# Performance work log

Measured on AMD Instinct MI355X. Metric: run time of the kernel, lower is better.

Reference implementation:

```python
import math
import jax, jax.numpy as jnp
import numpy as np

NUM_BUCKETS = 32
MAX_DISTANCE = 128
HEADS = 16
D_MODEL = 1024
SEQ = 1024
BATCH = 4
SCALE = (D_MODEL // HEADS) ** -0.5  # applied ONLY to the relative-position bias, per the source


def _rel_pos_bucket_causal(seq_len):
    """Causal T5 relative-position bucket: ret[i, j] for query i, key j."""
    pos = jnp.arange(seq_len)
    # rel_pos = k - q ; n = -rel_pos = q - k, clamped at 0 (causal branch)
    n = jnp.maximum(pos[:, None] - pos[None, :], 0)
    max_exact = NUM_BUCKETS // 2  # 16
    # log-spaced buckets for large distances; guard n>=1 to avoid log(0)
    val_large = max_exact + (
        jnp.log(jnp.maximum(n, 1).astype(jnp.float32) / max_exact)
        / math.log(MAX_DISTANCE / max_exact)
        * (NUM_BUCKETS - max_exact)
    ).astype(jnp.int32)
    val_large = jnp.minimum(val_large, NUM_BUCKETS - 1)
    return jnp.where(n < max_exact, n, val_large)  # [i, j] int32


def setup_inputs() -> dict:
    key = jax.random.key(0)
    ks = jax.random.split(key, 6)
    s = 0.02
    return {
        "x": jax.random.normal(ks[0], (BATCH, SEQ, D_MODEL), jnp.float32),
        "Wq": jax.random.normal(ks[1], (D_MODEL, D_MODEL), jnp.float32) * s,
        "bq": jnp.zeros((D_MODEL,), jnp.float32),
        "Wk": jax.random.normal(ks[2], (D_MODEL, D_MODEL), jnp.float32) * s,
        "bk": jnp.zeros((D_MODEL,), jnp.float32),
        "Wv": jax.random.normal(ks[3], (D_MODEL, D_MODEL), jnp.float32) * s,
        "bv": jnp.zeros((D_MODEL,), jnp.float32),
        "Wo": jax.random.normal(ks[4], (D_MODEL, D_MODEL), jnp.float32) * s,
        "bo": jnp.zeros((D_MODEL,), jnp.float32),
        "rel_emb": jax.random.normal(ks[5], (NUM_BUCKETS, HEADS), jnp.float32) * s,
    }


def reference(x, Wq, bq, Wk, bk, Wv, bv, Wo, bo, rel_emb):
    b, n, d = x.shape
    h, hd = HEADS, d // HEADS
    # projections (torch Linear: x @ W^T + b)
    q = (x @ Wq.T + bq).reshape(b, n, h, hd).transpose(0, 2, 1, 3)  # bhnd
    k = (x @ Wk.T + bk).reshape(b, n, h, hd).transpose(0, 2, 1, 3)
    v = (x @ Wv.T + bv).reshape(b, n, h, hd).transpose(0, 2, 1, 3)
    # unscaled dot-product scores (module does not scale q.k)
    sim = jnp.einsum("bhid,bhjd->bhij", q, k)
    # T5 relative-position bias, scaled by head_dim^-0.5
    rp_bucket = _rel_pos_bucket_causal(n)            # [i, j]
    bias = rel_emb[rp_bucket]                        # [i, j, h]
    sim = sim + jnp.transpose(bias, (2, 0, 1)) * SCALE  # broadcast over batch
    # additive causal mask (-inf above diagonal)
    i = jnp.arange(n)
    causal = jnp.where(i[None, :] > i[:, None], -jnp.inf, 0.0).astype(sim.dtype)
    sim = sim + causal
    attn = jax.nn.softmax(sim, axis=-1)
    out = jnp.einsum("bhij,bhjd->bhid", attn, v)
    out = out.transpose(0, 2, 1, 3).reshape(b, n, d)
    return out @ Wo.T + bo
```

## Files before the change

### kernel.cpp

```cpp
#include <hip/hip_runtime.h>
#include <hip/hip_bf16.h>
#include <stdint.h>

#define B_   4
#define SEQ_ 1024
#define DM   1024
#define H_   16
#define HD   64

typedef __bf16 bf16;
typedef __bf16 bf16x8 __attribute__((ext_vector_type(8)));
typedef __bf16 bf16x4v __attribute__((ext_vector_type(4)));
typedef __bf16 bf16x2 __attribute__((ext_vector_type(2)));
typedef float  f32x4 __attribute__((ext_vector_type(4)));

__device__ __forceinline__ void gl_lds16(const void* g, void* s_uniform) {
    __builtin_amdgcn_global_load_lds(
        (const __attribute__((address_space(1))) uint32_t*)g,
        (__attribute__((address_space(3))) uint32_t*)s_uniform,
        16, 0, 0);
}

__global__ __launch_bounds__(256) void prep_kernel(
    const float* __restrict__ x, const float* __restrict__ Wq,
    const float* __restrict__ Wk, const float* __restrict__ Wv,
    const float* __restrict__ Wo, const float* __restrict__ rel,
    bf16* __restrict__ xb, bf16* __restrict__ wqkvb, bf16* __restrict__ wob,
    float* __restrict__ biasT)
{
    int tid = blockIdx.x * 256 + threadIdx.x;
    int stride = gridDim.x * 256;

    for (int i = tid; i < (B_*SEQ_*DM)/4; i += stride) {
        float4 v = ((const float4*)x)[i];
        bf16x4v o; o[0]=(bf16)v.x; o[1]=(bf16)v.y; o[2]=(bf16)v.z; o[3]=(bf16)v.w;
        ((bf16x4v*)xb)[i] = o;
    }
    for (int i = tid; i < (3*DM*DM)/4; i += stride) {
        int n = i >> 8, k4 = i & 255;
        const float* src = (n < 1024) ? Wq : (n < 2048) ? Wk : Wv;
        float4 v = ((const float4*)(src + (size_t)(n & 1023) * DM))[k4];
        bf16x4v o; o[0]=(bf16)v.x; o[1]=(bf16)v.y; o[2]=(bf16)v.z; o[3]=(bf16)v.w;
        ((bf16x4v*)wqkvb)[i] = o;
    }
    for (int i = tid; i < (DM*DM)/4; i += stride) {
        float4 v = ((const float4*)Wo)[i];
        bf16x4v o; o[0]=(bf16)v.x; o[1]=(bf16)v.y; o[2]=(bf16)v.z; o[3]=(bf16)v.w;
        ((bf16x4v*)wob)[i] = o;
    }
    for (int i = tid; i < H_ * SEQ_; i += stride) {
        int h = i >> 10, dist = i & 1023;
        int bkt;
        if (dist < 16) {
            bkt = dist;
        } else {
            float r = logf((float)dist * (1.0f/16.0f)) / logf(8.0f) * 16.0f;
            int vb = 16 + (int)r;
            bkt = vb > 31 ? 31 : vb;
        }
        biasT[i] = rel[bkt * H_ + h] * 0.125f;
    }
}

template<int NT>
__global__ __launch_bounds__(256, 3) void gemm_ring(
    const bf16* __restrict__ Ag, const bf16* __restrict__ Bg,
    bf16* __restrict__ qb, bf16* __restrict__ kb, bf16* __restrict__ vtb,
    const float* __restrict__ bq, const float* __restrict__ bk,
    const float* __restrict__ bv)
{
    __shared__ __align__(16) bf16 tile[3][256 * 32];

    const int t = threadIdx.x;
    const int lane = t & 63, w = t >> 6;
    const int wr = w >> 1, wc = w & 1;
    const int row_l = lane & 15;
    const int lg = lane >> 4;

    int xcd = blockIdx.x & 7;
    int idx = blockIdx.x >> 3;
    int ty = (xcd >> 1) * 8 + idx / 12;
    int tx = (xcd & 1) * 12 + idx % 12;
    const int m0 = ty * 128, n0 = tx * 128;

    f32x4 acc[4][4] = {};

    auto STAGE = [&](int buf, int kt) {
        bf16* dst = &tile[buf][0];
        #pragma unroll
        for (int i = 0; i < 4; ++i) {
            int e = i * 2048 + t * 8;
            int r = e >> 5;
            int csw = ((t & 3) ^ (r & 3)) << 3;
            const bf16* src = (r < 128)
                ? (Ag + (long)(m0 + r) * 1024 + kt * 32 + csw)
                : (Bg + (long)(n0 + r - 128) * 1024 + kt * 32 + csw);
            gl_lds16(src, dst + i * 2048 + w * 512);
        }
    };

    auto COMPUTE = [&](int buf) {
        const bf16* bp = &tile[buf][0];
        bf16x8 af[4], bfr[4];
        #pragma unroll
        for (int m = 0; m < 4; ++m) {
            int ra = wr * 64 + m * 16 + row_l;
            af[m] = *(const bf16x8*)&bp[ra * 32 + ((lg ^ (ra & 3)) << 3)];
        }
        #pragma unroll
        for (int n = 0; n < 4; ++n) {
            int rb = 128 + wc * 64 + n * 16 + row_l;
            bfr[n] = *(const bf16x8*)&bp[rb * 32 + ((lg ^ (rb & 3)) << 3)];
        }
        #pragma unroll
        for (int m = 0; m < 4; ++m)
            #pragma unroll
            for (int n = 0; n < 4; ++n)
                acc[m][n] = __builtin_amdgcn_mfma_f32_16x16x32_bf16(
                    af[m], bfr[n], acc[m][n], 0, 0, 0);
    };

    STAGE(0, 0); STAGE(1, 1);
    asm volatile("s_waitcnt vmcnt(4)" ::: "memory");
    __builtin_amdgcn_s_barrier();

    int cb = 0;
    for (int kt = 0; kt < NT; ++kt) {
        int sb = cb - 1; if (sb < 0) sb += 3;
        if (kt + 2 < NT) STAGE(sb, kt + 2);
        COMPUTE(cb);
        if (kt + 2 < NT) { asm volatile("s_waitcnt vmcnt(4)" ::: "memory"); }
        else             { asm volatile("s_waitcnt vmcnt(0)" ::: "memory"); }
        __builtin_amdgcn_s_barrier();
        cb = (cb + 1 == 3) ? 0 : cb + 1;
    }

    const int rbase = (lane >> 4) * 4;

    if (n0 < 2048) {
        #pragma unroll
        for (int m = 0; m < 4; ++m) {
            #pragma unroll
            for (int n = 0; n < 4; ++n) {
                #pragma unroll
                for (int g = 0; g < 4; ++g) {
                    int gm = m0 + wr * 64 + m * 16 + rbase + g;
                    int gn = n0 + wc * 64 + n * 16 + row_l;
                    int which = gn >> 10, nn = gn & 1023;
                    int h = nn >> 6, d = nn & 63;
                    int b = gm >> 10, s = gm & 1023;
                    float v = acc[m][n][g] + ((which == 0) ? bq[nn] : bk[nn]);
                    bf16 bv16 = (bf16)v;
                    if (which == 0)
                        qb[((long)(b*H_ + h)*SEQ_ + s)*HD + d] = bv16;
                    else
                        kb[((long)(b*H_ + h)*SEQ_ + s)*HD + d] = bv16;
                }
            }
        }
    } else {
        bf16* lt = &tile[0][0];
        #pragma unroll
        for (int m = 0; m < 4; ++m) {
            #pragma unroll
            for (int n = 0; n < 4; ++n) {
                int nl = wc * 64 + n * 16 + row_l;
                int mlb = wr * 64 + m * 16 + rbase;
                float bvv = bv[(n0 & 1023) + nl];
                #pragma unroll
                for (int g2 = 0; g2 < 2; ++g2) {
                    bf16x2 pk;
                    pk[0] = (bf16)(acc[m][n][2*g2]     + bvv);
                    pk[1] = (bf16)(acc[m][n][2*g2 + 1] + bvv);
                    int ml = mlb + 2 * g2;
                    int byte = nl * 256 + ((ml * 2) ^ ((nl & 15) << 4));
                    *(bf16x2*)((char*)lt + byte) = pk;
                }
            }
        }
        __syncthreads();
        {
            int nl = t >> 1, sc = t & 1;
            int nn = (n0 & 1023) + nl;
            int h = nn >> 6, d = nn & 63;
            int b = m0 >> 10, s0 = (m0 & 1023) + sc * 64;
            bf16* dst = vtb + ((long)(b*H_ + h)*HD + d)*SEQ_ + s0;
            #pragma unroll
            for (int i = 0; i < 8; ++i) {
                int byte = nl * 256 + ((sc * 128 + i * 16) ^ ((nl & 15) << 4));
                *(float4*)(dst + i * 8) = *(const float4*)((char*)lt + byte);
            }
        }
    }
}

template<int NT>
__global__ __launch_bounds__(256, 2) void gemm_ring_o(
    const bf16* __restrict__ Ag, const bf16* __restrict__ Bg,
    float* __restrict__ outp, const float* __restrict__ bo)
{
    __shared__ __align__(16) bf16 tile[3][192 * 32];

    const int t = threadIdx.x;
    const int lane = t & 63, w = t >> 6;
    const int wr = w >> 1, wc = w & 1;
    const int row_l = lane & 15;
    const int lg = lane >> 4;

    int xcd = blockIdx.x & 7;
    int idx = blockIdx.x >> 3;
    int ty = (xcd >> 1) * 8 + (idx >> 3);
    int tx = (xcd & 1) * 8 + (idx & 7);
    const int m0 = ty * 128, n0 = tx * 64;

    f32x4 acc[4][2] = {};

    auto STAGE = [&](int buf, int kt) {
        bf16* dst = &tile[buf][0];
        #pragma unroll
        for (int i = 0; i < 3; ++i) {
            int e = i * 2048 + t * 8;
            int r = e >> 5;
            int csw = ((t & 3) ^ (r & 3)) << 3;
            const bf16* src = (r < 128)
                ? (Ag + (long)(m0 + r) * 1024 + kt * 32 + csw)
                : (Bg + (long)(n0 + r - 128) * 1024 + kt * 32 + csw);
            gl_lds16(src, dst + i * 2048 + w * 512);
        }
    };

    auto COMPUTE = [&](int buf) {
        const bf16* bp = &tile[buf][0];
        bf16x8 af[4], bfr[2];
        #pragma unroll
        for (int m = 0; m < 4; ++m) {
            int ra = wr * 64 + m * 16 + row_l;
            af[m] = *(const bf16x8*)&bp[ra * 32 + ((lg ^ (ra & 3)) << 3)];
        }
        #pragma unroll
        for (int n = 0; n < 2; ++n) {
            int rb = 128 + wc * 32 + n * 16 + row_l;
            bfr[n] = *(const bf16x8*)&bp[rb * 32 + ((lg ^ (rb & 3)) << 3)];
        }
        #pragma unroll
        for (int m = 0; m < 4; ++m)
            #pragma unroll
            for (int n = 0; n < 2; ++n)
                acc[m][n] = __builtin_amdgcn_mfma_f32_16x16x32_bf16(
                    af[m], bfr[n], acc[m][n], 0, 0, 0);
    };

    STAGE(0, 0); STAGE(1, 1);
    asm volatile("s_waitcnt vmcnt(3)" ::: "memory");
    __builtin_amdgcn_s_barrier();

    int cb = 0;
    for (int kt = 0; kt < NT; ++kt) {
        int sb = cb - 1; if (sb < 0) sb += 3;
        if (kt + 2 < NT) STAGE(sb, kt + 2);
        COMPUTE(cb);
        if (kt + 2 < NT) { asm volatile("s_waitcnt vmcnt(3)" ::: "memory"); }
        else             { asm volatile("s_waitcnt vmcnt(0)" ::: "memory"); }
        __builtin_amdgcn_s_barrier();
        cb = (cb + 1 == 3) ? 0 : cb + 1;
    }

    const int rbase = (lane >> 4) * 4;
    #pragma unroll
    for (int m = 0; m < 4; ++m) {
        #pragma unroll
        for (int n = 0; n < 2; ++n) {
            #pragma unroll
            for (int g = 0; g < 4; ++g) {
                int gm = m0 + wr * 64 + m * 16 + rbase + g;
                int gn = n0 + wc * 32 + n * 16 + row_l;
                outp[(long)gm * DM + gn] = acc[m][n][g] + bo[gn];
            }
        }
    }
}

#define PSTRIDE 72

__global__ __launch_bounds__(256, 3) void attn_kernel(
    const bf16* __restrict__ Qb, const bf16* __restrict__ Kb,
    const bf16* __restrict__ Vtb, const float* __restrict__ biasT,
    bf16* __restrict__ AO)
{
    __shared__ __align__(16) bf16 Ks[2][64 * 64];
    __shared__ __align__(16) bf16 Vs[2][64 * 64];
    __shared__ __align__(16) bf16 Ps[4][16 * PSTRIDE];
    __shared__ float biasS[SEQ_];

    int t = threadIdx.x;
    int lane = t & 63, w = t >> 6;

    int bid = blockIdx.x;
    int xcd = bid & 7;
    int widx = bid >> 3;
    int g = xcd * 8 + (widx >> 3);
    int pair = widx & 7;
    int qt_lo = pair, qt_hi = 15 - pair;
    int h = g & 15, b = g >> 4;

    int row_l = lane & 15;
    int ksl = (lane >> 4) * 8;
    int rbase = (lane >> 4) * 4;

    ((float4*)biasS)[t] = ((const float4*)(biasT + (long)h * SEQ_))[t];

    const bf16* Kbase = Kb + (long)g * SEQ_ * HD;
    const bf16* Vbase = Vtb + (long)g * HD * SEQ_;

    const bf16* QpA = Qb + ((long)g * SEQ_ + qt_lo * 64 + w * 16) * HD;
    const bf16* QpB = Qb + ((long)g * SEQ_ + qt_hi * 64 + w * 16) * HD;
    bf16x8 qA0 = *(const bf16x8*)&QpA[row_l * HD + ksl];
    bf16x8 qA1 = *(const bf16x8*)&QpA[row_l * HD + 32 + ksl];
    bf16x8 qB0 = *(const bf16x8*)&QpB[row_l * HD + ksl];
    bf16x8 qB1 = *(const bf16x8*)&QpB[row_l * HD + 32 + ksl];

    f32x4 oaccA[4] = {}, oaccB[4] = {};
    float lA[4] = {0.f, 0.f, 0.f, 0.f}, lB[4] = {0.f, 0.f, 0.f, 0.f};
    int irA[4], irB[4];
    #pragma unroll
    for (int q = 0; q < 4; ++q) {
        irA[q] = qt_lo * 64 + w * 16 + rbase + q;
        irB[q] = qt_hi * 64 + w * 16 + rbase + q;
    }

    int srow = w * 8 + (lane >> 3);
    int csw  = ((lane & 7) ^ (lane >> 3)) * 8;

    {
        int jt = 0;
        #pragma unroll
        for (int i = 0; i < 2; ++i) {
            int r = i * 32 + srow;
            gl_lds16(Kbase + (long)(jt*64 + r) * HD + csw, &Ks[0][i*2048 + w*512]);
            gl_lds16(Vbase + (long)r * SEQ_ + jt*64 + csw, &Vs[0][i*2048 + w*512]);
        }
    }
    __syncthreads();

    int cur = 0;
    for (int jt = 0; jt <= qt_hi; ++jt) {
        if (jt < qt_hi) {
            int nb = cur ^ 1, jn = jt + 1;
            #pragma unroll
            for (int i = 0; i < 2; ++i) {
                int r = i * 32 + srow;
                gl_lds16(Kbase + (long)(jn*64 + r) * HD + csw, &Ks[nb][i*2048 + w*512]);
                gl_lds16(Vbase + (long)r * SEQ_ + jn*64 + csw, &Vs[nb][i*2048 + w*512]);
            }
        }
        bool dolo = (jt <= qt_lo);

        f32x4 sA[4] = {}, sB[4] = {};
        __builtin_amdgcn_s_setprio(1);
        #pragma unroll
        for (int f = 0; f < 4; ++f) {
            int ra = f * 16 + row_l;
            int a0 = (ra * 64 + ksl)      ^ ((ra & 7) << 3);
            int a1 = (ra * 64 + 32 + ksl) ^ ((ra & 7) << 3);
            bf16x8 kf0 = *(const bf16x8*)&Ks[cur][a0];
            bf16x8 kf1 = *(const bf16x8*)&Ks[cur][a1];
            sB[f] = __builtin_amdgcn_mfma_f32_16x16x32_bf16(qB0, kf0, sB[f], 0,0,0);
            sB[f] = __builtin_amdgcn_mfma_f32_16x16x32_bf16(qB1, kf1, sB[f], 0,0,0);
            if (dolo) {
                sA[f] = __builtin_amdgcn_mfma_f32_16x16x32_bf16(qA0, kf0, sA[f], 0,0,0);
                sA[f] = __builtin_amdgcn_mfma_f32_16x16x32_bf16(qA1, kf1, sA[f], 0,0,0);
            }
        }
        __builtin_amdgcn_s_setprio(0);

        bf16x8 vf[4][2];
        #pragma unroll
        for (int f = 0; f < 4; ++f) {
            int ra = f * 16 + row_l;
            int a0 = (ra * 64 + ksl)      ^ ((ra & 7) << 3);
            int a1 = (ra * 64 + 32 + ksl) ^ ((ra & 7) << 3);
            vf[f][0] = *(const bf16x8*)&Vs[cur][a0];
            vf[f][1] = *(const bf16x8*)&Vs[cur][a1];
        }

        {
            #pragma unroll
            for (int f = 0; f < 4; ++f) {
                int j = jt * 64 + f * 16 + row_l;
                #pragma unroll
                for (int q = 0; q < 4; ++q) {
                    float sv = (j <= irB[q]) ? (sB[f][q] + biasS[irB[q] - j]) : -1e30f;
                    float p = __expf(sv);
                    lB[q] += p;
                    Ps[w][(rbase + q) * PSTRIDE + f * 16 + row_l] = (bf16)p;
                }
            }
            bf16x8 pf0 = *(const bf16x8*)&Ps[w][row_l * PSTRIDE + ksl];
            bf16x8 pf1 = *(const bf16x8*)&Ps[w][row_l * PSTRIDE + 32 + ksl];
            __builtin_amdgcn_s_setprio(1);
            #pragma unroll
            for (int db = 0; db < 4; ++db) {
                oaccB[db] = __builtin_amdgcn_mfma_f32_16x16x32_bf16(pf0, vf[db][0], oaccB[db], 0,0,0);
                oaccB[db] = __builtin_amdgcn_mfma_f32_16x16x32_bf16(pf1, vf[db][1], oaccB[db], 0,0,0);
            }
            __builtin_amdgcn_s_setprio(0);
        }

        if (dolo) {
            #pragma unroll
            for (int f = 0; f < 4; ++f) {
                int j = jt * 64 + f * 16 + row_l;
                #pragma unroll
                for (int q = 0; q < 4; ++q) {
                    float sv = (j <= irA[q]) ? (sA[f][q] + biasS[irA[q] - j]) : -1e30f;
                    float p = __expf(sv);
                    lA[q] += p;
                    Ps[w][(rbase + q) * PSTRIDE + f * 16 + row_l] = (bf16)p;
                }
            }
            bf16x8 pf0 = *(const bf16x8*)&Ps[w][row_l * PSTRIDE + ksl];
            bf16x8 pf1 = *(const bf16x8*)&Ps[w][row_l * PSTRIDE + 32 + ksl];
            __builtin_amdgcn_s_setprio(1);
            #pragma unroll
            for (int db = 0; db < 4; ++db) {
                oaccA[db] = __builtin_amdgcn_mfma_f32_16x16x32_bf16(pf0, vf[db][0], oaccA[db], 0,0,0);
                oaccA[db] = __builtin_amdgcn_mfma_f32_16x16x32_bf16(pf1, vf[db][1], oaccA[db], 0,0,0);
            }
            __builtin_amdgcn_s_setprio(0);
        }

        __syncthreads();
        cur ^= 1;
    }

    #pragma unroll
    for (int q = 0; q < 4; ++q) {
        float la = lA[q], lb = lB[q];
        #pragma unroll
        for (int off = 1; off < 16; off <<= 1) {
            la += __shfl_xor(la, off);
            lb += __shfl_xor(lb, off);
        }
        float invA = 1.0f / la;
        float invB = 1.0f / lb;
        long baseA = ((long)(b * SEQ_ + irA[q])) * DM + h * HD;
        long baseB = ((long)(b * SEQ_ + irB[q])) * DM + h * HD;
        #pragma unroll
        for (int db = 0; db < 4; ++db) {
            AO[baseA + db * 16 + row_l] = (bf16)(oaccA[db][q] * invA);
            AO[baseB + db * 16 + row_l] = (bf16)(oaccB[db][q] * invB);
        }
    }
}

extern "C" void kernel_launch(void* const* d_in, const int* in_sizes, int n_in,
                              void* d_out, int out_size, void* d_ws, size_t ws_size,
                              hipStream_t stream)
{
    const float* x   = (const float*)d_in[0];
    const float* Wq  = (const float*)d_in[1];
    const float* bq  = (const float*)d_in[2];
    const float* Wk  = (const float*)d_in[3];
    const float* bk  = (const float*)d_in[4];
    const float* Wv  = (const float*)d_in[5];
    const float* bv  = (const float*)d_in[6];
    const float* Wo  = (const float*)d_in[7];
    const float* bo  = (const float*)d_in[8];
    const float* rel = (const float*)d_in[9];
    float* out = (float*)d_out;

    char* ws = (char*)d_ws;
    bf16* xb    = (bf16*)ws;  ws += (size_t)B_*SEQ_*DM * 2;
    bf16* wqkvb = (bf16*)ws;  ws += (size_t)3*DM*DM * 2;
    bf16* wob   = (bf16*)ws;  ws += (size_t)DM*DM * 2;
    float* biasT= (float*)ws; ws += (size_t)H_*SEQ_ * 4;
    bf16* Qb    = (bf16*)ws;  ws += (size_t)B_*H_*SEQ_*HD * 2;
    bf16* Kb2   = (bf16*)ws;  ws += (size_t)B_*H_*SEQ_*HD * 2;
    bf16* Vtb   = (bf16*)ws;  ws += (size_t)B_*H_*SEQ_*HD * 2;
    bf16* AO    = (bf16*)ws;  ws += (size_t)B_*SEQ_*DM * 2;

    prep_kernel<<<2048, 256, 0, stream>>>(x, Wq, Wk, Wv, Wo, rel,
                                          xb, wqkvb, wob, biasT);

    gemm_ring<32><<<768, 256, 0, stream>>>(
        xb, wqkvb, Qb, Kb2, Vtb, bq, bk, bv);

    attn_kernel<<<512, 256, 0, stream>>>(Qb, Kb2, Vtb, biasT, AO);

    gemm_ring_o<32><<<512, 256, 0, stream>>>(AO, wob, out, bo);
}
```

Measured before the change: 100.6 us.

## Load K/V fragments directly from global into registers, drop LDS staging

Removes the double-buffered LDS staging of K and V tiles, which used global_load_lds with a prefetch and a per-iteration barrier. Each wave now loads its K and V MFMA fragments straight from global memory into registers every iteration, relying on L2/L1 to serve the fourfold redundant reads across the four waves. The per-tile __syncthreads is gone and LDS use drops, but there is no longer any prefetch, so load latency sits exposed at the start of each iteration. The launch-bounds occupancy hint also goes from 3 to 2 blocks per CU, which leaves room for the extra fragment registers.

```diff
diff --git a/kernel.cpp b/kernel.cpp
--- a/kernel.cpp
+++ b/kernel.cpp
@@ -282,13 +282,11 @@
 
 #define PSTRIDE 72
 
-__global__ __launch_bounds__(256, 3) void attn_kernel(
+__global__ __launch_bounds__(256, 2) void attn_kernel(
     const bf16* __restrict__ Qb, const bf16* __restrict__ Kb,
     const bf16* __restrict__ Vtb, const float* __restrict__ biasT,
     bf16* __restrict__ AO)
 {
-    __shared__ __align__(16) bf16 Ks[2][64 * 64];
-    __shared__ __align__(16) bf16 Vs[2][64 * 64];
     __shared__ __align__(16) bf16 Ps[4][16 * PSTRIDE];
     __shared__ float biasS[SEQ_];
 
@@ -308,6 +306,7 @@
     int rbase = (lane >> 4) * 4;
 
     ((float4*)biasS)[t] = ((const float4*)(biasT + (long)h * SEQ_))[t];
+    __syncthreads();
 
     const bf16* Kbase = Kb + (long)g * SEQ_ * HD;
     const bf16* Vbase = Vtb + (long)g * HD * SEQ_;
@@ -328,60 +327,32 @@
         irB[q] = qt_hi * 64 + w * 16 + rbase + q;
     }
 
-    int srow = w * 8 + (lane >> 3);
-    int csw  = ((lane & 7) ^ (lane >> 3)) * 8;
-
-    {
-        int jt = 0;
-        #pragma unroll
-        for (int i = 0; i < 2; ++i) {
-            int r = i * 32 + srow;
-            gl_lds16(Kbase + (long)(jt*64 + r) * HD + csw, &Ks[0][i*2048 + w*512]);
-            gl_lds16(Vbase + (long)r * SEQ_ + jt*64 + csw, &Vs[0][i*2048 + w*512]);
-        }
-    }
-    __syncthreads();
-
-    int cur = 0;
     for (int jt = 0; jt <= qt_hi; ++jt) {
-        if (jt < qt_hi) {
-            int nb = cur ^ 1, jn = jt + 1;
-            #pragma unroll
-            for (int i = 0; i < 2; ++i) {
-                int r = i * 32 + srow;
-                gl_lds16(Kbase + (long)(jn*64 + r) * HD + csw, &Ks[nb][i*2048 + w*512]);
-                gl_lds16(Vbase + (long)r * SEQ_ + jn*64 + csw, &Vs[nb][i*2048 + w*512]);
-            }
-        }
         bool dolo = (jt <= qt_lo);
+
+        bf16x8 kfr[4][2], vfr[4][2];
+        #pragma unroll
+        for (int f = 0; f < 4; ++f) {
+            const bf16* kp = Kbase + (long)(jt*64 + f*16 + row_l) * HD + ksl;
+            kfr[f][0] = *(const bf16x8*)kp;
+            kfr[f][1] = *(const bf16x8*)(kp + 32);
+            const bf16* vp = Vbase + (long)(f*16 + row_l) * SEQ_ + jt*64 + ksl;
+            vfr[f][0] = *(const bf16x8*)vp;
+            vfr[f][1] = *(const bf16x8*)(vp + 32);
+        }
 
         f32x4 sA[4] = {}, sB[4] = {};
         __builtin_amdgcn_s_setprio(1);
         #pragma unroll
         for (int f = 0; f < 4; ++f) {
-            int ra = f * 16 + row_l;
-            int a0 = (ra * 64 + ksl)      ^ ((ra & 7) << 3);
-            int a1 = (ra * 64 + 32 + ksl) ^ ((ra & 7) << 3);
-            bf16x8 kf0 = *(const bf16x8*)&Ks[cur][a0];
-            bf16x8 kf1 = *(const bf16x8*)&Ks[cur][a1];
-            sB[f] = __builtin_amdgcn_mfma_f32_16x16x32_bf16(qB0, kf0, sB[f], 0,0,0);
-            sB[f] = __builtin_amdgcn_mfma_f32_16x16x32_bf16(qB1, kf1, sB[f], 0,0,0);
+            sB[f] = __builtin_amdgcn_mfma_f32_16x16x32_bf16(qB0, kfr[f][0], sB[f], 0,0,0);
+            sB[f] = __builtin_amdgcn_mfma_f32_16x16x32_bf16(qB1, kfr[f][1], sB[f], 0,0,0);
             if (dolo) {
-                sA[f] = __builtin_amdgcn_mfma_f32_16x16x32_bf16(qA0, kf0, sA[f], 0,0,0);
-                sA[f] = __builtin_amdgcn_mfma_f32_16x16x32_bf16(qA1, kf1, sA[f], 0,0,0);
+                sA[f] = __builtin_amdgcn_mfma_f32_16x16x32_bf16(qA0, kfr[f][0], sA[f], 0,0,0);
+                sA[f] = __builtin_amdgcn_mfma_f32_16x16x32_bf16(qA1, kfr[f][1], sA[f], 0,0,0);
             }
         }
         __builtin_amdgcn_s_setprio(0);
-
-        bf16x8 vf[4][2];
-        #pragma unroll
-        for (int f = 0; f < 4; ++f) {
-            int ra = f * 16 + row_l;
-            int a0 = (ra * 64 + ksl)      ^ ((ra & 7) << 3);
-            int a1 = (ra * 64 + 32 + ksl) ^ ((ra & 7) << 3);
-            vf[f][0] = *(const bf16x8*)&Vs[cur][a0];
-            vf[f][1] = *(const bf16x8*)&Vs[cur][a1];
-        }
 
         {
             #pragma unroll
@@ -400,8 +371,8 @@
             __builtin_amdgcn_s_setprio(1);
             #pragma unroll
             for (int db = 0; db < 4; ++db) {
-                oaccB[db] = __builtin_amdgcn_mfma_f32_16x16x32_bf16(pf0, vf[db][0], oaccB[db], 0,0,0);
-                oaccB[db] = __builtin_amdgcn_mfma_f32_16x16x32_bf16(pf1, vf[db][1], oaccB[db], 0,0,0);
+                oaccB[db] = __builtin_amdgcn_mfma_f32_16x16x32_bf16(pf0, vfr[db][0], oaccB[db], 0,0,0);
+                oaccB[db] = __builtin_amdgcn_mfma_f32_16x16x32_bf16(pf1, vfr[db][1], oaccB[db], 0,0,0);
             }
             __builtin_amdgcn_s_setprio(0);
         }
@@ -423,14 +394,11 @@
             __builtin_amdgcn_s_setprio(1);
             #pragma unroll
             for (int db = 0; db < 4; ++db) {
-                oaccA[db] = __builtin_amdgcn_mfma_f32_16x16x32_bf16(pf0, vf[db][0], oaccA[db], 0,0,0);
-                oaccA[db] = __builtin_amdgcn_mfma_f32_16x16x32_bf16(pf1, vf[db][1], oaccA[db], 0,0,0);
+                oaccA[db] = __builtin_amdgcn_mfma_f32_16x16x32_bf16(pf0, vfr[db][0], oaccA[db], 0,0,0);
+                oaccA[db] = __builtin_amdgcn_mfma_f32_16x16x32_bf16(pf1, vfr[db][1], oaccA[db], 0,0,0);
             }
             __builtin_amdgcn_s_setprio(0);
         }
-
-        __syncthreads();
-        cur ^= 1;
     }
 
     #pragma unroll
```

Result: slower. 126.1 us (+25.4%).
